# Kernel optimization log

Measured on AMD Instinct MI355X. Metric: run time of the kernel, lower is better.

## Reference

```python
import jax, jax.numpy as jnp
import numpy as np
import math

D_MODEL = 512
NUM_CLASSES = 8
MEM_SLOTS = 64
STEPS = 4
DECAY = 0.9
TOPK = 8
SCORE_CLIP = 10.0
VOCAB = 32000
MAX_LEN = 2048
B, T = 32, 2048


def _linear_params(key, d_in, d_out):
    kw, kb = jax.random.split(key)
    W = jax.random.normal(kw, (d_in, d_out), jnp.float32) * (1.0 / math.sqrt(d_in))
    b = jnp.zeros((d_out,), jnp.float32)
    return W, b


def setup_inputs() -> dict:
    key = jax.random.key(0)
    ks = jax.random.split(key, 16)
    inp = {}
    inp["input_ids"] = jax.random.randint(ks[0], (B, T), 0, VOCAB)
    inp["attention_mask"] = jnp.ones((B, T), jnp.int32)
    inp["token_emb"] = jax.random.normal(ks[1], (VOCAB, D_MODEL), jnp.float32) * 0.02
    inp["pos_emb"] = jax.random.normal(ks[2], (MAX_LEN, D_MODEL), jnp.float32) * 0.02
    inp["memory_init"] = jax.random.normal(ks[3], (1, MEM_SLOTS, D_MODEL), jnp.float32) * 0.02
    names = ["q", "k", "v", "write", "gate", "rq", "rk", "rv"]
    for i, n in enumerate(names):
        W, b = _linear_params(ks[4 + i], D_MODEL, D_MODEL)
        inp[n + "_W"], inp[n + "_b"] = W, b
    inp["fuse_W"], inp["fuse_b"] = _linear_params(ks[12], 2 * D_MODEL, D_MODEL)
    inp["cls_W"], inp["cls_b"] = _linear_params(ks[13], D_MODEL, NUM_CLASSES)
    inp["tln_g"] = jnp.ones((D_MODEL,), jnp.float32)
    inp["tln_b"] = jnp.zeros((D_MODEL,), jnp.float32)
    inp["mln_g"] = jnp.ones((D_MODEL,), jnp.float32)
    inp["mln_b"] = jnp.zeros((D_MODEL,), jnp.float32)
    return inp


def _layer_norm(x, g, b, eps=1e-5):
    mu = jnp.mean(x, axis=-1, keepdims=True)
    var = jnp.var(x, axis=-1, keepdims=True)
    return (x - mu) * jax.lax.rsqrt(var + eps) * g + b


def _topk_softmax(scores, k):
    # scores: (B, T, S). Equivalent to scatter top-k vals into -inf then softmax:
    # softmax over the top-k entries, zeros elsewhere.
    Bb, Tt, S = scores.shape
    tv, ti = jax.lax.top_k(scores, k)           # (B,T,k)
    w = jax.nn.softmax(tv, axis=-1)
    rows = jnp.arange(Bb * Tt)[:, None]
    out = jnp.zeros((Bb * Tt, S), scores.dtype).at[rows, ti.reshape(-1, k)].set(w.reshape(-1, k))
    return out.reshape(Bb, Tt, S)


def _binding(scores, mask_f, k):
    w = _topk_softmax(jnp.clip(scores, -SCORE_CLIP, SCORE_CLIP), k)
    w = w * mask_f
    return w / jnp.maximum(jnp.sum(w, axis=-1, keepdims=True), 1e-9)


def _forward(input_ids, attention_mask, token_emb, pos_emb, memory_init,
             q_W, q_b, k_W, k_b, v_W, v_b, write_W, write_b, gate_W, gate_b,
             rq_W, rq_b, rk_W, rk_b, rv_W, rv_b, fuse_W, fuse_b,
             cls_W, cls_b, tln_g, tln_b, mln_g, mln_b):
    scale = 1.0 / math.sqrt(D_MODEL)
    tokens = token_emb[input_ids] + pos_emb[jnp.arange(input_ids.shape[1])][None]
    tokens = _layer_norm(tokens, tln_g, tln_b)  # (B,T,D)
    mask_f = attention_mask[..., None].astype(tokens.dtype)  # (B,T,1)
    memory = jnp.broadcast_to(memory_init, (input_ids.shape[0], MEM_SLOTS, D_MODEL))
    for _ in range(STEPS):
        q = tokens @ q_W + q_b
        kk = memory @ k_W + k_b
        scores = jnp.einsum("btd,bsd->bts", q, kk) * scale
        binding = _binding(scores, mask_f, TOPK)  # (B,T,S)
        v = tokens @ v_W + v_b
        write = jnp.einsum("bts,btd->bsd", binding, v)
        slot_usage = jnp.maximum(jnp.sum(binding, axis=1)[..., None], 1e-6)  # (B,S,1)
        write = (write / slot_usage) @ write_W + write_b
        write = jax.nn.sigmoid(write @ gate_W + gate_b) * write
        memory = _layer_norm(DECAY * memory + (1.0 - DECAY) * write, mln_g, mln_b)
    # read
    rq = tokens @ rq_W + rq_b
    rk = memory @ rk_W + rk_b
    rv = memory @ rv_W + rv_b
    scores = jnp.einsum("btd,bsd->bts", rq, rk) * scale
    rw = _binding(scores, mask_f, TOPK)
    context = jnp.einsum("bts,bsd->btd", rw, rv)
    fused = jnp.concatenate([tokens, context], axis=-1) @ fuse_W + fuse_b
    pooled = jnp.sum(fused * mask_f, axis=1) / jnp.maximum(jnp.sum(mask_f, axis=1), 1.0)
    return pooled @ cls_W + cls_b  # (B, C)


def reference(input_ids, attention_mask, token_emb, pos_emb, memory_init,
              q_W, q_b, k_W, k_b, v_W, v_b, write_W, write_b, gate_W, gate_b,
              rq_W, rq_b, rk_W, rk_b, rv_W, rv_b, fuse_W, fuse_b,
              cls_W, cls_b, tln_g, tln_b, mln_g, mln_b):
    return _forward(input_ids, attention_mask, token_emb, pos_emb, memory_init,
                    q_W, q_b, k_W, k_b, v_W, v_b, write_W, write_b, gate_W, gate_b,
                    rq_W, rq_b, rk_W, rk_b, rv_W, rv_b, fuse_W, fuse_b,
                    cls_W, cls_b, tln_g, tln_b, mln_g, mln_b)
```

## Files before the change

kernel.cpp:

```cpp
#include <hip/hip_runtime.h>
#include <hip/hip_bf16.h>
#include <math.h>

#define BB 32
#define TT 2048
#define DM 512
#define SS 64
#define BT (BB*TT)
#define NSTEPS 4
#define SCALE 0.044194173824159216f

typedef unsigned short u16;
typedef unsigned int u32;
typedef __attribute__((ext_vector_type(8))) short s16x8;
typedef __attribute__((ext_vector_type(4))) float f32x4;
typedef __attribute__((ext_vector_type(4))) unsigned u32x4;

__device__ __forceinline__ u16 f2b(float x){
  __hip_bfloat16 h = __float2bfloat16(x);
  return *reinterpret_cast<u16*>(&h);
}
__device__ __forceinline__ float b2f(u16 u){
  __hip_bfloat16 h;
  *reinterpret_cast<u16*>(&h) = u;
  return __bfloat162float(h);
}

static __device__ __forceinline__ float wave_reduce_sum(float v){
  #pragma unroll
  for (int off=32; off; off>>=1) v += __shfl_down(v, off);
  return v;
}

__global__ __launch_bounds__(256) void embed_ln_k(const int* __restrict__ ids,
    const float* __restrict__ temb, const float* __restrict__ pemb,
    const float* __restrict__ g, const float* __restrict__ be, u16* __restrict__ out){
  int row = blockIdx.x;
  int t = row & (TT-1);
  int id = ids[row];
  int d = threadIdx.x;
  const float* te = temb + (size_t)id*DM;
  const float* pe = pemb + (size_t)t*DM;
  float x0 = te[d] + pe[d];
  float x1 = te[d+256] + pe[d+256];
  float s1 = x0+x1, s2 = x0*x0 + x1*x1;
  s1 = wave_reduce_sum(s1); s2 = wave_reduce_sum(s2);
  __shared__ float r1[4], r2[4];
  int lane = d & 63, w = d>>6;
  if (lane==0){ r1[w]=s1; r2[w]=s2; }
  __syncthreads();
  float S1 = r1[0]+r1[1]+r1[2]+r1[3];
  float S2 = r2[0]+r2[1]+r2[2]+r2[3];
  float mu = S1 * (1.f/DM);
  float var = S2*(1.f/DM) - mu*mu;
  float rs = rsqrtf(var + 1e-5f);
  u16* orow = out + (size_t)row*DM;
  orow[d]     = f2b((x0-mu)*rs*g[d] + be[d]);
  orow[d+256] = f2b((x1-mu)*rs*g[d+256] + be[d+256]);
}

template<int EPI>
__global__ __launch_bounds__(128) void ntgemm_k(const u16* __restrict__ A,
    const u16* __restrict__ Bm, const float* __restrict__ bias,
    const u16* __restrict__ mulb, const float* __restrict__ rowv,
    void* __restrict__ Cout, float scalep){
  int m0 = blockIdx.x*32 + (threadIdx.x>>6)*16;
  int n0 = blockIdx.y*64;
  int l = threadIdx.x & 63;
  int lr = l & 15, lk = (l>>4)*8;
  const u16* Arow = A + (size_t)(m0 + lr)*512 + lk;
  const u16* B0   = Bm + (size_t)(n0 + lr)*512 + lk;
  f32x4 acc[4] = {};
  #pragma unroll
  for (int k0=0;k0<512;k0+=32){
    s16x8 a = *(const s16x8*)(Arow + k0);
    #pragma unroll
    for (int j=0;j<4;j++){
      s16x8 b = *(const s16x8*)(B0 + (size_t)j*16*512 + k0);
      acc[j] = __builtin_amdgcn_mfma_f32_16x16x32_bf16(a, b, acc[j], 0,0,0);
    }
  }
  int mbase = m0 + (l>>4)*4;
  #pragma unroll
  for (int j=0;j<4;j++){
    int n = n0 + j*16 + lr;
    #pragma unroll
    for (int r=0;r<4;r++){
      int m = mbase + r;
      float v = acc[j][r];
      if (EPI==0){ ((u16*)Cout)[(size_t)m*512 + n] = f2b(v + bias[n]); }
      if (EPI==1){ ((u16*)Cout)[(size_t)m*512 + n] = f2b(v + rowv[m]*bias[n]); }
      if (EPI==2){
        float z = v + bias[n];
        float sg = 1.f/(1.f + expf(-z));
        ((float*)Cout)[(size_t)m*512 + n] = b2f(mulb[(size_t)m*512 + n]) * sg;
      }
      if (EPI==3){ ((float*)Cout)[(size_t)m*512 + n] = v + bias[n]; }
      if (EPI==4){ ((u16*)Cout)[(size_t)m*512 + n] = f2b(v * scalep); }
    }
  }
}

__global__ __launch_bounds__(64) void bind_k(const u16* __restrict__ tok,
    const u16* __restrict__ Pt, const float* __restrict__ cbuf, const int* __restrict__ mask,
    u16* __restrict__ BNDT, float* __restrict__ cspart){
  int b = blockIdx.y, t0 = blockIdx.x*64;
  int l = threadIdx.x;
  int lr = l&15, g = l>>4, lk = g*8;
  __shared__ float sc[64*66];
  __shared__ u16 bt[64*66];

  const u16* Abase = tok + ((size_t)(b*TT + t0 + lr))*512 + lk;
  const u16* Bbase = Pt + ((size_t)(b*SS + lr))*512 + lk;
  f32x4 acc[4][4] = {};
  #pragma unroll
  for (int k0=0;k0<512;k0+=32){
    s16x8 a[4], bb[4];
    #pragma unroll
    for (int mi=0;mi<4;mi++) a[mi] = *(const s16x8*)(Abase + (size_t)mi*16*512 + k0);
    #pragma unroll
    for (int nj=0;nj<4;nj++) bb[nj] = *(const s16x8*)(Bbase + (size_t)nj*16*512 + k0);
    #pragma unroll
    for (int mi=0;mi<4;mi++)
      #pragma unroll
      for (int nj=0;nj<4;nj++)
        acc[mi][nj] = __builtin_amdgcn_mfma_f32_16x16x32_bf16(a[mi], bb[nj], acc[mi][nj], 0,0,0);
  }
  float cbv[4];
  #pragma unroll
  for (int nj=0;nj<4;nj++) cbv[nj] = cbuf[b*SS + 16*nj + lr];
  #pragma unroll
  for (int mi=0;mi<4;mi++)
    #pragma unroll
    for (int nj=0;nj<4;nj++)
      #pragma unroll
      for (int r=0;r<4;r++){
        float x = acc[mi][nj][r] + cbv[nj];
        x = fminf(fmaxf(x, -10.f), 10.f);
        sc[(16*mi + 4*g + r)*66 + 16*nj + lr] = x;
      }

  float sv[64];
  #pragma unroll
  for (int j=0;j<64;j++) sv[j] = sc[l*66 + j];

  u32 work[64];
  #pragma unroll
  for (int j=0;j<64;j++){
    u32 s = __float_as_uint(sv[j]);
    u32 o = s ^ ((u32)(((int)s) >> 31) | 0x80000000u);
    work[j] = (o & 0xFFFFFFC0u) | (u32)(63 - j);
  }
  u32 mtop = 0;
  #pragma unroll
  for (int it=0; it<8; ++it){
    u32 a[32];
    #pragma unroll
    for (int j=0;j<32;j++){ u32 x = work[2*j], y = work[2*j+1]; a[j] = x>y?x:y; }
    #pragma unroll
    for (int lvl=16; lvl>=1; lvl>>=1)
      #pragma unroll
      for (int j=0;j<lvl;j++){ u32 x = a[2*j], y = a[2*j+1]; a[j] = x>y?x:y; }
    u32 m = a[0];
    if (it==0) mtop = m;
    #pragma unroll
    for (int j=0;j<64;j++) work[j] = (work[j]==m) ? 0u : work[j];
  }
  u32 ot = mtop & 0xFFFFFFC0u;
  u32 tb = (ot & 0x80000000u) ? (ot ^ 0x80000000u) : ~ot;
  float T = __uint_as_float(tb);

  float tot = 0.f;
  #pragma unroll
  for (int j=0;j<64;j++){
    float ej = (work[j]==0u) ? expf(sv[j]-T) : 0.f;
    sv[j] = ej;
    tot += ej;
  }
  int mv = mask[b*TT + t0 + l];
  float inv = mv ? 1.f/tot : 0.f;
  #pragma unroll
  for (int j=0;j<64;j++)
    bt[j*66 + l] = f2b(sv[j]*inv);

  const u32* btw = (const u32*)bt;
  u32 rowbuf[32];
  float csum = 0.f;
  #pragma unroll
  for (int w=0;w<32;w++){
    u32 v = btw[l*33 + w];
    rowbuf[w] = v;
    csum += b2f((u16)(v & 0xFFFFu)) + b2f((u16)(v >> 16));
  }
  cspart[((size_t)b*32 + blockIdx.x)*64 + l] = csum;
  u16* dst = BNDT + ((size_t)(b*SS + l))*TT + t0;
  #pragma unroll
  for (int w8=0;w8<8;w8++){
    u32x4 v;
    v[0]=rowbuf[4*w8]; v[1]=rowbuf[4*w8+1]; v[2]=rowbuf[4*w8+2]; v[3]=rowbuf[4*w8+3];
    *(u32x4*)(dst + 8*w8) = v;
  }
}

__global__ __launch_bounds__(64) void csred_k(const float* __restrict__ cspart,
    float* __restrict__ slot, float* __restrict__ rr, float* __restrict__ raw){
  int b = blockIdx.x, s = threadIdx.x;
  float t = 0.f;
  for (int k=0;k<32;k++) t += cspart[((size_t)b*32 + k)*64 + s];
  raw[b*SS+s] = t;
  float sl = fmaxf(t, 1e-6f);
  slot[b*SS+s] = sl;
  rr[b*SS+s] = t/sl;
}

__global__ __launch_bounds__(256) void wt_k(const u16* __restrict__ BNDT,
    const u16* __restrict__ tok, float* __restrict__ part){
  int dgrp = blockIdx.x, b = blockIdx.y, ks = blockIdx.z;
  int tid = threadIdx.x, w = tid>>6, l = tid&63;
  int lr = l&15, lk = (l>>4)*8;
  __shared__ u16 tk[128][72];
  f32x4 acc[8] = {};
  int trow = tid>>2, dseg = (tid&3)*32;
  const u16* tokbase = tok + ((size_t)b*TT)*512 + dgrp*128;
  const u16* Abase = BNDT + ((size_t)(b*SS + 16*w + lr))*TT;
  for (int chunk=0; chunk<8; ++chunk){
    int tb = ks*512 + chunk*64;
    const u16* src = tokbase + (size_t)(tb + trow)*512 + dseg;
    s16x8 v0 = *(const s16x8*)(src);
    s16x8 v1 = *(const s16x8*)(src+8);
    s16x8 v2 = *(const s16x8*)(src+16);
    s16x8 v3 = *(const s16x8*)(src+24);
    #pragma unroll
    for (int e=0;e<8;e++){
      int d0 = dseg+e, d1 = dseg+8+e, d2 = dseg+16+e, d3 = dseg+24+e;
      tk[d0][(trow + 8*((d0>>5)&3)) & 63] = (u16)v0[e];
      tk[d1][(trow + 8*((d1>>5)&3)) & 63] = (u16)v1[e];
      tk[d2][(trow + 8*((d2>>5)&3)) & 63] = (u16)v2[e];
      tk[d3][(trow + 8*((d3>>5)&3)) & 63] = (u16)v3[e];
    }
    __syncthreads();
    #pragma unroll
    for (int kst=0;kst<2;kst++){
      s16x8 a = *(const s16x8*)(Abase + tb + kst*32 + lk);
      #pragma unroll
      for (int nt=0;nt<8;nt++){
        int dd = nt*16 + lr;
        int cb2 = (kst*32 + lk + 8*((dd>>5)&3)) & 63;
        s16x8 bb = *(const s16x8*)&tk[dd][cb2];
        acc[nt] = __builtin_amdgcn_mfma_f32_16x16x32_bf16(a, bb, acc[nt], 0,0,0);
      }
    }
    __syncthreads();
  }
  float* dst = part + (size_t)ks*2048*512 + ((size_t)(b*SS))*512 + dgrp*128;
  #pragma unroll
  for (int nt=0;nt<8;nt++){
    int d = nt*16 + lr;
    #pragma unroll
    for (int r=0;r<4;r++){
      int s = 16*w + (l>>4)*4 + r;
      dst[(size_t)s*512 + d] = acc[nt][r];
    }
  }
}

__global__ __launch_bounds__(256) void wtred_k(const float* __restrict__ part,
    const float* __restrict__ slot, u16* __restrict__ t1h){
  int i = blockIdx.x*256 + threadIdx.x;
  int row = i>>9;
  float v = part[i] + part[i + 2048*512] + part[i + 2*2048*512] + part[i + 3*2048*512];
  t1h[i] = f2b(v / slot[row]);
}

__global__ __launch_bounds__(256) void cb_k(const float* __restrict__ mem,
    const float* __restrict__ wcb, const float* __restrict__ cb0p, float* __restrict__ cb){
  int row = blockIdx.x*4 + (threadIdx.x>>6), l = threadIdx.x&63;
  const float* r = mem + (size_t)row*512;
  float s = 0.f;
  #pragma unroll
  for (int k=0;k<8;k++) s += r[l + 64*k]*wcb[l + 64*k];
  #pragma unroll
  for (int off=32; off; off>>=1) s += __shfl_xor(s, off);
  if (l==0) cb[row] = s + cb0p[0];
}

__global__ __launch_bounds__(256) void matvec_k(const float* __restrict__ W,
    const float* __restrict__ v, float* __restrict__ out){
  int i = blockIdx.x*4 + (threadIdx.x>>6), l = threadIdx.x&63;
  const float* r = W + (size_t)i*512;
  float s = 0.f;
  #pragma unroll
  for (int k=0;k<8;k++) s += r[l + 64*k]*v[l + 64*k];
  #pragma unroll
  for (int off=32; off; off>>=1) s += __shfl_xor(s, off);
  if (l==0) out[i] = s * SCALE;
}

__global__ __launch_bounds__(128) void dot2_k(const float* __restrict__ a0, const float* __restrict__ b0,
    const float* __restrict__ a1, const float* __restrict__ b1, float* __restrict__ out){
  int w = threadIdx.x>>6, l = threadIdx.x&63;
  const float* a = w ? a1 : a0;
  const float* b = w ? b1 : b0;
  float s = 0.f;
  #pragma unroll
  for (int k=0;k<8;k++) s += a[l + 64*k]*b[l + 64*k];
  #pragma unroll
  for (int off=32; off; off>>=1) s += __shfl_xor(s, off);
  if (l==0) out[w] = s * SCALE;
}

__global__ __launch_bounds__(256) void tconv_k(const float* __restrict__ in, u16* __restrict__ out){
  __shared__ float t[32][33];
  int c0 = blockIdx.x*32, r0 = blockIdx.y*32;
  int cx = threadIdx.x&31, ry = threadIdx.x>>5;
  #pragma unroll
  for (int i=0;i<4;i++){ int r = ry + i*8; t[r][cx] = in[(size_t)(r0+r)*512 + c0+cx]; }
  __syncthreads();
  #pragma unroll
  for (int i=0;i<4;i++){ int r = ry + i*8; out[(size_t)(c0+r)*512 + r0+cx] = f2b(t[cx][r]); }
}

__global__ __launch_bounds__(256) void conv_k(const float* __restrict__ in, u16* __restrict__ out){
  int i = blockIdx.x*256 + threadIdx.x;
  out[i] = f2b(in[i]);
}

__global__ __launch_bounds__(256) void meminit_k(const float* __restrict__ src,
    float* __restrict__ mem, u16* __restrict__ memh){
  int i = blockIdx.x*256 + threadIdx.x;
  float v = src[i & (SS*DM-1)];
  mem[i] = v;
  memh[i] = f2b(v);
}

__global__ __launch_bounds__(256) void mem_ln_k(float* __restrict__ mem, const float* __restrict__ w3,
    const float* __restrict__ g, const float* __restrict__ be, u16* __restrict__ memh){
  int row = blockIdx.x;
  int d = threadIdx.x;
  float* mrow = mem + (size_t)row*DM;
  const float* wrow = w3 + (size_t)row*DM;
  float x0 = 0.9f*mrow[d]     + 0.1f*wrow[d];
  float x1 = 0.9f*mrow[d+256] + 0.1f*wrow[d+256];
  float s1 = x0+x1, s2 = x0*x0 + x1*x1;
  s1 = wave_reduce_sum(s1); s2 = wave_reduce_sum(s2);
  __shared__ float r1[4], r2[4];
  int lane = d & 63, w = d>>6;
  if (lane==0){ r1[w]=s1; r2[w]=s2; }
  __syncthreads();
  float S1 = r1[0]+r1[1]+r1[2]+r1[3];
  float S2 = r2[0]+r2[1]+r2[2]+r2[3];
  float mu = S1 * (1.f/DM);
  float var = S2*(1.f/DM) - mu*mu;
  float rs = rsqrtf(var + 1e-5f);
  float y0 = (x0-mu)*rs*g[d] + be[d];
  float y1 = (x1-mu)*rs*g[d+256] + be[d+256];
  mrow[d] = y0; mrow[d+256] = y1;
  memh[(size_t)row*DM + d] = f2b(y0);
  memh[(size_t)row*DM + d+256] = f2b(y1);
}

__global__ __launch_bounds__(256) void tokpart_k(const u16* __restrict__ tok,
    const int* __restrict__ mask, float* __restrict__ tp){
  int b = blockIdx.x, sl = blockIdx.y;
  int w = threadIdx.x>>6, l = threadIdx.x&63;
  float acc[8] = {};
  #pragma unroll 4
  for (int i=0;i<32;i++){
    int t = sl*128 + w + 4*i;
    float m = (float)mask[b*TT + t];
    s16x8 v = *(const s16x8*)(tok + ((size_t)(b*TT + t))*512 + l*8);
    #pragma unroll
    for (int e=0;e<8;e++) acc[e] += m*b2f((u16)v[e]);
  }
  float* dst = tp + ((size_t)(b*64 + sl*4 + w))*512 + l*8;
  #pragma unroll
  for (int e=0;e<8;e++) dst[e] = acc[e];
}

__global__ __launch_bounds__(256) void catden_k(const float* __restrict__ tp,
    const float* __restrict__ rws, const float* __restrict__ rv,
    const int* __restrict__ mask, float* __restrict__ cat, float* __restrict__ denomv){
  int b = blockIdx.x, tid = threadIdx.x;
  float dn = 0.f;
  for (int t=tid; t<TT; t+=256) dn += (float)mask[b*TT+t];
  dn = wave_reduce_sum(dn);
  __shared__ float dred[4];
  if ((tid&63)==0) dred[tid>>6]=dn;
  #pragma unroll
  for (int it=0; it<2; ++it){
    int d = tid + it*256;
    float ts = 0.f;
    for (int k=0;k<64;k++) ts += tp[((size_t)(b*64+k))*512 + d];
    cat[(size_t)b*1024 + d] = ts;
    float c = 0.f;
    for (int s=0;s<SS;s++) c += rws[b*SS+s]*rv[((size_t)b*SS+s)*DM + d];
    cat[(size_t)b*1024 + 512 + d] = c;
  }
  __syncthreads();
  if (tid==0) denomv[b] = dred[0]+dred[1]+dred[2]+dred[3];
}

__global__ __launch_bounds__(256) void fuse_k(const float* __restrict__ cat,
    const float* __restrict__ denomv, const float* __restrict__ fuseW,
    const float* __restrict__ fuseb, float* __restrict__ pooled){
  int b = blockIdx.x, n0 = blockIdx.y*64;
  int l = threadIdx.x&63, kc = threadIdx.x>>6;
  int n = n0 + l;
  float acc = 0.f;
  const float* crow = cat + (size_t)b*1024;
  for (int k=kc*256; k<kc*256+256; ++k)
    acc += crow[k]*fuseW[(size_t)k*512 + n];
  __shared__ float red[4][64];
  red[kc][l] = acc;
  __syncthreads();
  if (kc==0){
    float denom = denomv[b];
    float tot = red[0][l]+red[1][l]+red[2][l]+red[3][l];
    pooled[(size_t)b*512 + n] = (tot + denom*fuseb[n]) / fmaxf(denom, 1.f);
  }
}

__global__ __launch_bounds__(256) void cls_k(const float* __restrict__ pooled,
    const float* __restrict__ clsW, const float* __restrict__ clsb, float* __restrict__ out){
  int b = blockIdx.x;
  int c = threadIdx.x&7, kc = threadIdx.x>>3;
  float acc = 0.f;
  const float* prow = pooled + (size_t)b*512;
  for (int d=kc*16; d<kc*16+16; ++d) acc += prow[d]*clsW[d*8+c];
  __shared__ float red[32][8];
  red[kc][c] = acc;
  __syncthreads();
  if (threadIdx.x < 8){
    float tot = 0.f;
    #pragma unroll
    for (int k=0;k<32;k++) tot += red[k][threadIdx.x];
    out[b*8 + threadIdx.x] = tot + clsb[threadIdx.x];
  }
}

extern "C" void kernel_launch(void* const* d_in, const int* in_sizes, int n_in,
                              void* d_out, int out_size, void* d_ws, size_t ws_size,
                              hipStream_t stream){
  (void)in_sizes; (void)n_in; (void)out_size; (void)ws_size;
  const int*   ids   = (const int*)d_in[0];
  const int*   amask = (const int*)d_in[1];
  const float* temb  = (const float*)d_in[2];
  const float* pemb  = (const float*)d_in[3];
  const float* mem0  = (const float*)d_in[4];
  const float* qW=(const float*)d_in[5],  *qB=(const float*)d_in[6];
  const float* kW=(const float*)d_in[7],  *kB=(const float*)d_in[8];
  const float* vW=(const float*)d_in[9],  *vB=(const float*)d_in[10];
  const float* wrW=(const float*)d_in[11],*wrB=(const float*)d_in[12];
  const float* gtW=(const float*)d_in[13],*gtB=(const float*)d_in[14];
  const float* rqW=(const float*)d_in[15],*rqB=(const float*)d_in[16];
  const float* rkW=(const float*)d_in[17],*rkB=(const float*)d_in[18];
  const float* rvW=(const float*)d_in[19],*rvB=(const float*)d_in[20];
  const float* fW=(const float*)d_in[21], *fB=(const float*)d_in[22];
  const float* cW=(const float*)d_in[23], *cB=(const float*)d_in[24];
  const float* tg=(const float*)d_in[25], *tb=(const float*)d_in[26];
  const float* mg=(const float*)d_in[27], *mb=(const float*)d_in[28];

  char* p = (char*)d_ws;
  size_t off = 0;
  auto alloc = [&](size_t bytes)->char*{ char* r = p + off; off += (bytes + 255) & ~(size_t)255; return r; };
  u16*   tokens = (u16*)  alloc((size_t)BT*DM*2);
  u16*   Pt     = (u16*)  alloc((size_t)BB*SS*DM*2);
  u16*   BNDT   = (u16*)  alloc((size_t)BB*SS*TT*2);
  float* cspart = (float*)alloc((size_t)BB*32*64*4);
  float* wtpart = (float*)alloc((size_t)4*2048*512*4);
  u16*   t1h    = (u16*)  alloc((size_t)2048*512*2);
  u16*   t2h    = (u16*)  alloc((size_t)2048*512*2);
  u16*   zh     = (u16*)  alloc((size_t)2048*512*2);
  float* mem    = (float*)alloc((size_t)BB*SS*DM*4);
  u16*   memh   = (u16*)  alloc((size_t)BB*SS*DM*2);
  u16*   vWT    = (u16*)  alloc(512*512*2);
  u16*   wrWT   = (u16*)  alloc(512*512*2);
  u16*   gtWT   = (u16*)  alloc(512*512*2);
  u16*   rvWT   = (u16*)  alloc(512*512*2);
  u16*   WqkT   = (u16*)  alloc(512*512*2);
  u16*   WqkT_r = (u16*)  alloc(512*512*2);
  float* bq     = (float*)alloc(512*4);
  float* bq_r   = (float*)alloc(512*4);
  float* wcb    = (float*)alloc(512*4);
  float* wcb_r  = (float*)alloc(512*4);
  float* cb0s   = (float*)alloc(256);
  float* cbuf   = (float*)alloc(2048*4);
  float* slot   = (float*)alloc(2048*4);
  float* rr     = (float*)alloc(2048*4);
  float* raw    = (float*)alloc(2048*4);
  float* catbuf = (float*)alloc((size_t)BB*1024*4);
  float* denomv = (float*)alloc(BB*4);
  float* pooled = (float*)alloc((size_t)BB*512*4);
  float* rv32   = wtpart;
  float* tspart = wtpart + 1048576;
  float* gh32   = wtpart + 2097152;
  u16*   qWb    = (u16*)((char*)wtpart + 12582912);
  u16*   kWb    = qWb + 512*512;
  u16*   rqWb   = kWb + 512*512;
  u16*   rkWb   = rqWb + 512*512;

  conv_k<<<1024, 256, 0, stream>>>(qW, qWb);
  conv_k<<<1024, 256, 0, stream>>>(kW, kWb);
  conv_k<<<1024, 256, 0, stream>>>(rqW, rqWb);
  conv_k<<<1024, 256, 0, stream>>>(rkW, rkWb);
  tconv_k<<<dim3(16,16), 256, 0, stream>>>(vW, vWT);
  tconv_k<<<dim3(16,16), 256, 0, stream>>>(wrW, wrWT);
  tconv_k<<<dim3(16,16), 256, 0, stream>>>(gtW, gtWT);
  tconv_k<<<dim3(16,16), 256, 0, stream>>>(rvW, rvWT);
  ntgemm_k<4><<<dim3(16,8), 128, 0, stream>>>(qWb, kWb, nullptr, nullptr, nullptr, WqkT, SCALE);
  ntgemm_k<4><<<dim3(16,8), 128, 0, stream>>>(rqWb, rkWb, nullptr, nullptr, nullptr, WqkT_r, SCALE);
  matvec_k<<<128, 256, 0, stream>>>(qW, kB, bq);
  matvec_k<<<128, 256, 0, stream>>>(rqW, rkB, bq_r);
  matvec_k<<<128, 256, 0, stream>>>(kW, qB, wcb);
  matvec_k<<<128, 256, 0, stream>>>(rkW, rqB, wcb_r);
  dot2_k<<<1, 128, 0, stream>>>(kB, qB, rkB, rqB, cb0s);
  embed_ln_k<<<BT, 256, 0, stream>>>(ids, temb, pemb, tg, tb, tokens);
  meminit_k<<<(BB*SS*DM)/256, 256, 0, stream>>>(mem0, mem, memh);

  for (int step=0; step<NSTEPS; ++step){
    ntgemm_k<0><<<dim3(64,8), 128, 0, stream>>>(memh, WqkT, bq, nullptr, nullptr, Pt, 0.f);
    cb_k<<<512, 256, 0, stream>>>(mem, wcb, cb0s, cbuf);
    bind_k<<<dim3(32,32), 64, 0, stream>>>(tokens, Pt, cbuf, amask, BNDT, cspart);
    csred_k<<<32, 64, 0, stream>>>(cspart, slot, rr, raw);
    wt_k<<<dim3(4,32,4), 256, 0, stream>>>(BNDT, tokens, wtpart);
    wtred_k<<<4096, 256, 0, stream>>>(wtpart, slot, t1h);
    ntgemm_k<1><<<dim3(64,8), 128, 0, stream>>>(t1h, vWT, vB, nullptr, rr, t2h, 0.f);
    ntgemm_k<0><<<dim3(64,8), 128, 0, stream>>>(t2h, wrWT, wrB, nullptr, nullptr, zh, 0.f);
    ntgemm_k<2><<<dim3(64,8), 128, 0, stream>>>(zh, gtWT, gtB, zh, nullptr, gh32, 0.f);
    mem_ln_k<<<BB*SS, 256, 0, stream>>>(mem, gh32, mg, mb, memh);
  }

  ntgemm_k<0><<<dim3(64,8), 128, 0, stream>>>(memh, WqkT_r, bq_r, nullptr, nullptr, Pt, 0.f);
  cb_k<<<512, 256, 0, stream>>>(mem, wcb_r, cb0s+1, cbuf);
  bind_k<<<dim3(32,32), 64, 0, stream>>>(tokens, Pt, cbuf, amask, BNDT, cspart);
  csred_k<<<32, 64, 0, stream>>>(cspart, slot, rr, raw);
  ntgemm_k<3><<<dim3(64,8), 128, 0, stream>>>(memh, rvWT, rvB, nullptr, nullptr, rv32, 0.f);
  tokpart_k<<<dim3(32,16), 256, 0, stream>>>(tokens, amask, tspart);
  catden_k<<<32, 256, 0, stream>>>(tspart, raw, rv32, amask, catbuf, denomv);
  fuse_k<<<dim3(32,8), 256, 0, stream>>>(catbuf, denomv, fW, fB, pooled);
  cls_k<<<32, 256, 0, stream>>>(pooled, cW, cB, (float*)d_out);
}
```

Measured before the change: 623.5 us.

## Precompose value and write projections into one weight; vectorize embed layernorm

```diff
diff --git a/kernel.cpp b/kernel.cpp
--- a/kernel.cpp
+++ b/kernel.cpp
@@ -35,35 +35,41 @@
 __global__ __launch_bounds__(256) void embed_ln_k(const int* __restrict__ ids,
     const float* __restrict__ temb, const float* __restrict__ pemb,
     const float* __restrict__ g, const float* __restrict__ be, u16* __restrict__ out){
-  int row = blockIdx.x;
+  int row = blockIdx.x*4 + (threadIdx.x>>6);
+  int l = threadIdx.x & 63;
   int t = row & (TT-1);
   int id = ids[row];
-  int d = threadIdx.x;
-  const float* te = temb + (size_t)id*DM;
-  const float* pe = pemb + (size_t)t*DM;
-  float x0 = te[d] + pe[d];
-  float x1 = te[d+256] + pe[d+256];
-  float s1 = x0+x1, s2 = x0*x0 + x1*x1;
-  s1 = wave_reduce_sum(s1); s2 = wave_reduce_sum(s2);
-  __shared__ float r1[4], r2[4];
-  int lane = d & 63, w = d>>6;
-  if (lane==0){ r1[w]=s1; r2[w]=s2; }
-  __syncthreads();
-  float S1 = r1[0]+r1[1]+r1[2]+r1[3];
-  float S2 = r2[0]+r2[1]+r2[2]+r2[3];
-  float mu = S1 * (1.f/DM);
-  float var = S2*(1.f/DM) - mu*mu;
+  const float* te = temb + (size_t)id*DM + l*8;
+  const float* pe = pemb + (size_t)t*DM + l*8;
+  float4 a0 = *(const float4*)te,     a1 = *(const float4*)(te+4);
+  float4 p0 = *(const float4*)pe,     p1 = *(const float4*)(pe+4);
+  float x[8] = {a0.x+p0.x, a0.y+p0.y, a0.z+p0.z, a0.w+p0.w,
+                a1.x+p1.x, a1.y+p1.y, a1.z+p1.z, a1.w+p1.w};
+  float s1 = 0.f, s2 = 0.f;
+  #pragma unroll
+  for (int e=0;e<8;e++){ s1 += x[e]; s2 += x[e]*x[e]; }
+  #pragma unroll
+  for (int off=1; off<64; off<<=1){ s1 += __shfl_xor(s1, off); s2 += __shfl_xor(s2, off); }
+  float mu = s1*(1.f/DM);
+  float var = s2*(1.f/DM) - mu*mu;
   float rs = rsqrtf(var + 1e-5f);
-  u16* orow = out + (size_t)row*DM;
-  orow[d]     = f2b((x0-mu)*rs*g[d] + be[d]);
-  orow[d+256] = f2b((x1-mu)*rs*g[d+256] + be[d+256]);
+  const float* gp = g + l*8;
+  const float* bp = be + l*8;
+  float4 g0=*(const float4*)gp, g1=*(const float4*)(gp+4);
+  float4 b0=*(const float4*)bp, b1=*(const float4*)(bp+4);
+  float gg[8]={g0.x,g0.y,g0.z,g0.w,g1.x,g1.y,g1.z,g1.w};
+  float bb[8]={b0.x,b0.y,b0.z,b0.w,b1.x,b1.y,b1.z,b1.w};
+  s16x8 o;
+  #pragma unroll
+  for (int e=0;e<8;e++) o[e] = (short)f2b((x[e]-mu)*rs*gg[e] + bb[e]);
+  *(s16x8*)(out + (size_t)row*DM + l*8) = o;
 }
 
 template<int EPI>
 __global__ __launch_bounds__(128) void ntgemm_k(const u16* __restrict__ A,
     const u16* __restrict__ Bm, const float* __restrict__ bias,
     const u16* __restrict__ mulb, const float* __restrict__ rowv,
-    void* __restrict__ Cout, float scalep){
+    const float* __restrict__ bias2, void* __restrict__ Cout, float scalep){
   int m0 = blockIdx.x*32 + (threadIdx.x>>6)*16;
   int n0 = blockIdx.y*64;
   int l = threadIdx.x & 63;
@@ -89,7 +95,6 @@
       int m = mbase + r;
       float v = acc[j][r];
       if (EPI==0){ ((u16*)Cout)[(size_t)m*512 + n] = f2b(v + bias[n]); }
-      if (EPI==1){ ((u16*)Cout)[(size_t)m*512 + n] = f2b(v + rowv[m]*bias[n]); }
       if (EPI==2){
         float z = v + bias[n];
         float sg = 1.f/(1.f + expf(-z));
@@ -97,6 +102,7 @@
       }
       if (EPI==3){ ((float*)Cout)[(size_t)m*512 + n] = v + bias[n]; }
       if (EPI==4){ ((u16*)Cout)[(size_t)m*512 + n] = f2b(v * scalep); }
+      if (EPI==5){ ((u16*)Cout)[(size_t)m*512 + n] = f2b(v + rowv[m]*bias[n] + bias2[n]); }
     }
   }
 }
@@ -294,6 +300,14 @@
   #pragma unroll
   for (int off=32; off; off>>=1) s += __shfl_xor(s, off);
   if (l==0) out[i] = s * SCALE;
+}
+
+__global__ __launch_bounds__(256) void matvecc_k(const float* __restrict__ W,
+    const float* __restrict__ v, float* __restrict__ out){
+  int n = blockIdx.x*256 + threadIdx.x;
+  float s = 0.f;
+  for (int o=0;o<512;o++) s += v[o]*W[(size_t)o*512 + n];
+  out[n] = s;
 }
 
 __global__ __launch_bounds__(128) void dot2_k(const float* __restrict__ a0, const float* __restrict__ b0,
@@ -469,20 +483,20 @@
   float* cspart = (float*)alloc((size_t)BB*32*64*4);
   float* wtpart = (float*)alloc((size_t)4*2048*512*4);
   u16*   t1h    = (u16*)  alloc((size_t)2048*512*2);
-  u16*   t2h    = (u16*)  alloc((size_t)2048*512*2);
   u16*   zh     = (u16*)  alloc((size_t)2048*512*2);
   float* mem    = (float*)alloc((size_t)BB*SS*DM*4);
   u16*   memh   = (u16*)  alloc((size_t)BB*SS*DM*2);
-  u16*   vWT    = (u16*)  alloc(512*512*2);
   u16*   wrWT   = (u16*)  alloc(512*512*2);
   u16*   gtWT   = (u16*)  alloc(512*512*2);
   u16*   rvWT   = (u16*)  alloc(512*512*2);
   u16*   WqkT   = (u16*)  alloc(512*512*2);
   u16*   WqkT_r = (u16*)  alloc(512*512*2);
+  u16*   WvwT   = (u16*)  alloc(512*512*2);
   float* bq     = (float*)alloc(512*4);
   float* bq_r   = (float*)alloc(512*4);
   float* wcb    = (float*)alloc(512*4);
   float* wcb_r  = (float*)alloc(512*4);
+  float* bvw    = (float*)alloc(512*4);
   float* cb0s   = (float*)alloc(256);
   float* cbuf   = (float*)alloc(2048*4);
   float* slot   = (float*)alloc(2048*4);
@@ -498,43 +512,45 @@
   u16*   kWb    = qWb + 512*512;
   u16*   rqWb   = kWb + 512*512;
   u16*   rkWb   = rqWb + 512*512;
+  u16*   vWb    = (u16*)((char*)wtpart + 14680064);
 
   conv_k<<<1024, 256, 0, stream>>>(qW, qWb);
   conv_k<<<1024, 256, 0, stream>>>(kW, kWb);
   conv_k<<<1024, 256, 0, stream>>>(rqW, rqWb);
   conv_k<<<1024, 256, 0, stream>>>(rkW, rkWb);
-  tconv_k<<<dim3(16,16), 256, 0, stream>>>(vW, vWT);
+  conv_k<<<1024, 256, 0, stream>>>(vW, vWb);
   tconv_k<<<dim3(16,16), 256, 0, stream>>>(wrW, wrWT);
   tconv_k<<<dim3(16,16), 256, 0, stream>>>(gtW, gtWT);
   tconv_k<<<dim3(16,16), 256, 0, stream>>>(rvW, rvWT);
-  ntgemm_k<4><<<dim3(16,8), 128, 0, stream>>>(qWb, kWb, nullptr, nullptr, nullptr, WqkT, SCALE);
-  ntgemm_k<4><<<dim3(16,8), 128, 0, stream>>>(rqWb, rkWb, nullptr, nullptr, nullptr, WqkT_r, SCALE);
+  ntgemm_k<4><<<dim3(16,8), 128, 0, stream>>>(qWb, kWb, nullptr, nullptr, nullptr, nullptr, WqkT, SCALE);
+  ntgemm_k<4><<<dim3(16,8), 128, 0, stream>>>(rqWb, rkWb, nullptr, nullptr, nullptr, nullptr, WqkT_r, SCALE);
+  ntgemm_k<4><<<dim3(16,8), 128, 0, stream>>>(wrWT, vWb, nullptr, nullptr, nullptr, nullptr, WvwT, 1.0f);
   matvec_k<<<128, 256, 0, stream>>>(qW, kB, bq);
   matvec_k<<<128, 256, 0, stream>>>(rqW, rkB, bq_r);
   matvec_k<<<128, 256, 0, stream>>>(kW, qB, wcb);
   matvec_k<<<128, 256, 0, stream>>>(rkW, rqB, wcb_r);
+  matvecc_k<<<2, 256, 0, stream>>>(wrW, vB, bvw);
   dot2_k<<<1, 128, 0, stream>>>(kB, qB, rkB, rqB, cb0s);
-  embed_ln_k<<<BT, 256, 0, stream>>>(ids, temb, pemb, tg, tb, tokens);
+  embed_ln_k<<<BT/4, 256, 0, stream>>>(ids, temb, pemb, tg, tb, tokens);
   meminit_k<<<(BB*SS*DM)/256, 256, 0, stream>>>(mem0, mem, memh);
 
   for (int step=0; step<NSTEPS; ++step){
-    ntgemm_k<0><<<dim3(64,8), 128, 0, stream>>>(memh, WqkT, bq, nullptr, nullptr, Pt, 0.f);
+    ntgemm_k<0><<<dim3(64,8), 128, 0, stream>>>(memh, WqkT, bq, nullptr, nullptr, nullptr, Pt, 0.f);
     cb_k<<<512, 256, 0, stream>>>(mem, wcb, cb0s, cbuf);
     bind_k<<<dim3(32,32), 64, 0, stream>>>(tokens, Pt, cbuf, amask, BNDT, cspart);
     csred_k<<<32, 64, 0, stream>>>(cspart, slot, rr, raw);
     wt_k<<<dim3(4,32,4), 256, 0, stream>>>(BNDT, tokens, wtpart);
     wtred_k<<<4096, 256, 0, stream>>>(wtpart, slot, t1h);
-    ntgemm_k<1><<<dim3(64,8), 128, 0, stream>>>(t1h, vWT, vB, nullptr, rr, t2h, 0.f);
-    ntgemm_k<0><<<dim3(64,8), 128, 0, stream>>>(t2h, wrWT, wrB, nullptr, nullptr, zh, 0.f);
-    ntgemm_k<2><<<dim3(64,8), 128, 0, stream>>>(zh, gtWT, gtB, zh, nullptr, gh32, 0.f);
+    ntgemm_k<5><<<dim3(64,8), 128, 0, stream>>>(t1h, WvwT, bvw, nullptr, rr, wrB, zh, 0.f);
+    ntgemm_k<2><<<dim3(64,8), 128, 0, stream>>>(zh, gtWT, gtB, zh, nullptr, nullptr, gh32, 0.f);
     mem_ln_k<<<BB*SS, 256, 0, stream>>>(mem, gh32, mg, mb, memh);
   }
 
-  ntgemm_k<0><<<dim3(64,8), 128, 0, stream>>>(memh, WqkT_r, bq_r, nullptr, nullptr, Pt, 0.f);
+  ntgemm_k<0><<<dim3(64,8), 128, 0, stream>>>(memh, WqkT_r, bq_r, nullptr, nullptr, nullptr, Pt, 0.f);
   cb_k<<<512, 256, 0, stream>>>(mem, wcb_r, cb0s+1, cbuf);
   bind_k<<<dim3(32,32), 64, 0, stream>>>(tokens, Pt, cbuf, amask, BNDT, cspart);
   csred_k<<<32, 64, 0, stream>>>(cspart, slot, rr, raw);
-  ntgemm_k<3><<<dim3(64,8), 128, 0, stream>>>(memh, rvWT, rvB, nullptr, nullptr, rv32, 0.f);
+  ntgemm_k<3><<<dim3(64,8), 128, 0, stream>>>(memh, rvWT, rvB, nullptr, nullptr, nullptr, rv32, 0.f);
   tokpart_k<<<dim3(32,16), 256, 0, stream>>>(tokens, amask, tspart);
   catden_k<<<32, 256, 0, stream>>>(tspart, raw, rv32, amask, catbuf, denomv);
   fuse_k<<<dim3(32,8), 256, 0, stream>>>(catbuf, denomv, fW, fB, pooled);
```

New measurement: 586.1 us. 1.06x faster.
